# Performance work log

Hardware: AMD Instinct MI355X
Metric: run time of the kernel (lower is better)

The kernel has to match this reference:

```python
import jax, jax.numpy as jnp
import numpy as np

BATCH = 16384
IN_DIM = 256
UNITS = 256


def setup_inputs() -> dict:
    key = jax.random.key(0)
    ks = jax.random.split(key, 5)
    scale = 1.0 / np.sqrt(IN_DIM + UNITS)
    return {
        "x": jax.random.normal(ks[0], (BATCH, IN_DIM), dtype=jnp.float32),
        "prev_h": jax.random.normal(ks[1], (BATCH, UNITS), dtype=jnp.float32),
        "Wz": jax.random.normal(ks[2], (IN_DIM + UNITS, UNITS), dtype=jnp.float32) * scale,
        "bz": jnp.zeros((UNITS,), dtype=jnp.float32),
        "Wr": jax.random.normal(ks[3], (IN_DIM + UNITS, UNITS), dtype=jnp.float32) * scale,
        "br": jnp.zeros((UNITS,), dtype=jnp.float32),
        "Ws": jax.random.normal(ks[4], (IN_DIM + UNITS, UNITS), dtype=jnp.float32) * scale,
        "bs": jnp.zeros((UNITS,), dtype=jnp.float32),
    }


def reference(x, prev_h, Wz, bz, Wr, br, Ws, bs):
    # concat order matches the TF module: [prev_h, x]
    concat = jnp.concatenate([prev_h, x], axis=1)  # [B, units+in_dim]
    z = jax.nn.sigmoid(concat @ Wz + bz)
    r = jax.nn.sigmoid(concat @ Wr + br)
    concat_cand = jnp.concatenate([r * prev_h, x], axis=1)
    h_tilda = jnp.tanh(concat_cand @ Ws + bs)
    h_new = (1.0 - z) * prev_h + z * h_tilda
    return h_new
```

## Files before the change

kernel.cpp:

```cpp
#include <hip/hip_runtime.h>
#include <hip/hip_bf16.h>


#define ROWS 64

typedef float f32x4 __attribute__((ext_vector_type(4)));
typedef __bf16 bf16x8 __attribute__((ext_vector_type(8)));
typedef unsigned short us8 __attribute__((ext_vector_type(8)));
typedef unsigned short us4v __attribute__((ext_vector_type(4)));

static __device__ __forceinline__ unsigned short f2bf(float f) {
    __bf16 h = (__bf16)f;
    return __builtin_bit_cast(unsigned short, h);
}
static __device__ __forceinline__ float bf2f(unsigned short u) {
    union { unsigned u; float f; } v; v.u = ((unsigned)u) << 16;
    return v.f;
}

__global__ void pack_weights(const float* __restrict__ Wz,
                             const float* __restrict__ Wr,
                             const float* __restrict__ Ws,
                             unsigned short* __restrict__ out) {
    int gid = blockIdx.x * blockDim.x + threadIdx.x;
    int w    = gid >> 14;
    int rem  = gid & 16383;
    int kt   = rem >> 10;
    int rem2 = rem & 1023;
    int nt   = rem2 >> 6;
    int lane = rem2 & 63;
    int hi = lane >> 4, lo = lane & 15;
    const float* W = (w == 0) ? Wz : (w == 1) ? Wr : Ws;
    const float* src = W + (size_t)(kt * 32 + hi * 8) * 256 + nt * 16 + lo;
    us8 o;
#pragma unroll
    for (int j = 0; j < 8; ++j) o[j] = f2bf(src[(size_t)j * 256]);
    *(us8*)&out[(size_t)w * 131072 + (size_t)(((kt * 16 + nt) * 64 + lane) * 8)] = o;
}

__launch_bounds__(1024, 4)
__global__ void gru_main(const float* __restrict__ x,
                         const float* __restrict__ ph,
                         const float* __restrict__ bz,
                         const float* __restrict__ br,
                         const float* __restrict__ bs,
                         const unsigned short* __restrict__ Wp,
                         float* __restrict__ out) {
    __shared__ unsigned short sm[ROWS * 512];
    __shared__ unsigned short rh[ROWS * 256];

    const int tid  = threadIdx.x;
    const int lane = tid & 63;
    const int wid  = tid >> 6;
    const int brow = blockIdx.x * ROWS;

    const int l15 = lane & 15;
    const int kg  = (lane >> 4) << 3;
    const int col = wid * 16 + l15;

    const unsigned short* pz = Wp          + (size_t)((wid * 64 + lane) * 8);
    const unsigned short* pr = Wp + 131072 + (size_t)((wid * 64 + lane) * 8);
    const unsigned short* ps = Wp + 262144 + (size_t)((wid * 64 + lane) * 8);
    us8 b0n = *(const us8*)pz;
    us8 b1n = *(const us8*)pr;
    float bzc = bz[col], brc = br[col], bsc = bs[col];

#pragma unroll
    for (int it = 0; it < 4; ++it) {
        int i   = tid + it * 1024;
        int row = i >> 6;
        int c4  = (i & 63) << 2;
        int swr = (row & 7) << 3;
        float4 a = *(const float4*)&ph[(size_t)(brow + row) * 256 + c4];
        us4v u; u.x = f2bf(a.x); u.y = f2bf(a.y); u.z = f2bf(a.z); u.w = f2bf(a.w);
        *(us4v*)&sm[row * 512 + (c4 ^ swr)] = u;
    }
    __syncthreads();

    float4 xr[4];
#pragma unroll
    for (int it = 0; it < 4; ++it) {
        int i   = tid + it * 1024;
        int row = i >> 6;
        int c4  = (i & 63) << 2;
        xr[it] = *(const float4*)&x[(size_t)(brow + row) * 256 + c4];
    }

    f32x4 accz[4] = {};
    f32x4 accr[4] = {};
#pragma unroll 4
    for (int kt = 0; kt < 8; ++kt) {
        bf16x8 B0 = __builtin_bit_cast(bf16x8, b0n);
        bf16x8 B1 = __builtin_bit_cast(bf16x8, b1n);
        b0n = *(const us8*)(pz + (size_t)(kt + 1) * 8192);
        b1n = *(const us8*)(pr + (size_t)(kt + 1) * 8192);
        int ak = kt * 32 + kg;
#pragma unroll
        for (int m = 0; m < 4; ++m) {
            int arow = m * 16 + l15;
            bf16x8 a = __builtin_bit_cast(bf16x8,
                *(const us8*)&sm[arow * 512 + (ak ^ ((arow & 7) << 3))]);
            accz[m] = __builtin_amdgcn_mfma_f32_16x16x32_bf16(a, B0, accz[m], 0, 0, 0);
            accr[m] = __builtin_amdgcn_mfma_f32_16x16x32_bf16(a, B1, accr[m], 0, 0, 0);
        }
    }

#pragma unroll
    for (int it = 0; it < 4; ++it) {
        int i   = tid + it * 1024;
        int row = i >> 6;
        int c4  = (i & 63) << 2;
        int swr = (row & 7) << 3;
        us4v v; v.x = f2bf(xr[it].x); v.y = f2bf(xr[it].y);
        v.z = f2bf(xr[it].z); v.w = f2bf(xr[it].w);
        *(us4v*)&sm[row * 512 + ((256 + c4) ^ swr)] = v;
    }
    __syncthreads();

    us8 s0n = *(const us8*)(ps + (size_t)8 * 8192);
    us8 s1n = *(const us8*)(ps + (size_t)9 * 8192);

    f32x4 accs[4] = {};
#pragma unroll 4
    for (int kt = 8; kt < 16; ++kt) {
        bf16x8 B0 = __builtin_bit_cast(bf16x8, b0n);
        bf16x8 B1 = __builtin_bit_cast(bf16x8, b1n);
        bf16x8 S  = __builtin_bit_cast(bf16x8, s0n);
        s0n = s1n;
        if (kt < 15) {
            size_t no = (size_t)(kt + 1) * 8192;
            b0n = *(const us8*)(pz + no);
            b1n = *(const us8*)(pr + no);
        }
        if (kt < 14) s1n = *(const us8*)(ps + (size_t)(kt + 2) * 8192);
        int ak = kt * 32 + kg;
#pragma unroll
        for (int m = 0; m < 4; ++m) {
            int arow = m * 16 + l15;
            bf16x8 a = __builtin_bit_cast(bf16x8,
                *(const us8*)&sm[arow * 512 + (ak ^ ((arow & 7) << 3))]);
            accz[m] = __builtin_amdgcn_mfma_f32_16x16x32_bf16(a, B0, accz[m], 0, 0, 0);
            accr[m] = __builtin_amdgcn_mfma_f32_16x16x32_bf16(a, B1, accr[m], 0, 0, 0);
            accs[m] = __builtin_amdgcn_mfma_f32_16x16x32_bf16(a, S,  accs[m], 0, 0, 0);
        }
    }

    s0n = *(const us8*)ps;
    s1n = *(const us8*)(ps + 8192);

    float pst[4][4];
    const int rrow0 = (lane >> 4) * 4;
#pragma unroll
    for (int m = 0; m < 4; ++m) {
#pragma unroll
        for (int i = 0; i < 4; ++i) {
            int lrow = m * 16 + rrow0 + i;
            int cs = col ^ ((lrow & 7) << 3);
            float p = bf2f(sm[lrow * 512 + cs]);
            float z = 1.f / (1.f + __expf(-(accz[m][i] + bzc)));
            float r = 1.f / (1.f + __expf(-(accr[m][i] + brc)));
            accz[m][i] = z;
            pst[m][i]  = p;
            rh[lrow * 256 + cs] = f2bf(r * p);
        }
    }
    __syncthreads();

#pragma unroll 4
    for (int kt = 0; kt < 8; ++kt) {
        bf16x8 B = __builtin_bit_cast(bf16x8, s0n);
        s0n = s1n;
        if (kt < 6) s1n = *(const us8*)(ps + (size_t)(kt + 2) * 8192);
        int ak = kt * 32 + kg;
#pragma unroll
        for (int m = 0; m < 4; ++m) {
            int arow = m * 16 + l15;
            bf16x8 a = __builtin_bit_cast(bf16x8,
                *(const us8*)&rh[arow * 256 + (ak ^ ((arow & 7) << 3))]);
            accs[m] = __builtin_amdgcn_mfma_f32_16x16x32_bf16(a, B, accs[m], 0, 0, 0);
        }
    }

#pragma unroll
    for (int m = 0; m < 4; ++m) {
#pragma unroll
        for (int i = 0; i < 4; ++i) {
            float s = accs[m][i] + bsc;
            float e = __expf(-2.f * fabsf(s));
            float th = (1.f - e) / (1.f + e);
            th = (s < 0.f) ? -th : th;
            float z = accz[m][i];
            float p = pst[m][i];
            int grow = brow + m * 16 + rrow0 + i;
            out[(size_t)grow * 256 + col] = (1.f - z) * p + z * th;
        }
    }
}

extern "C" void kernel_launch(void* const* d_in, const int* in_sizes, int n_in,
                              void* d_out, int out_size, void* d_ws, size_t ws_size,
                              hipStream_t stream) {
    const float* x  = (const float*)d_in[0];
    const float* ph = (const float*)d_in[1];
    const float* Wz = (const float*)d_in[2];
    const float* bz = (const float*)d_in[3];
    const float* Wr = (const float*)d_in[4];
    const float* br = (const float*)d_in[5];
    const float* Ws = (const float*)d_in[6];
    const float* bs = (const float*)d_in[7];
    unsigned short* Wp = (unsigned short*)d_ws;

    hipLaunchKernelGGL(pack_weights, dim3(192), dim3(256), 0, stream, Wz, Wr, Ws, Wp);
    hipLaunchKernelGGL(gru_main, dim3(256), dim3(1024), 0, stream,
                       x, ph, bz, br, bs, Wp, (float*)d_out);
}
```

Measured before the change: 33.80 us.

## Halve row tile to 32 and give each wave two column tiles

The block tile drops from 64 to 32 rows, with 512 threads instead of 1024 and twice as many blocks. Each of the 8 waves now covers 32 output columns as two 16-column MFMA tiles, so every A fragment read from LDS feeds twice as many MFMAs. Weight prefetch is restructured to load both column tiles per k-step. This gives more blocks and better A reuse, at the cost of more weight traffic per output row and more accumulator registers per thread. The shared arrays are still sized with ROWS, so LDS use per block halves.

```diff
diff --git a/kernel.cpp b/kernel.cpp
--- a/kernel.cpp
+++ b/kernel.cpp
@@ -2,7 +2,7 @@
 #include <hip/hip_bf16.h>
 
 
-#define ROWS 64
+#define ROWS 32
 
 typedef float f32x4 __attribute__((ext_vector_type(4)));
 typedef __bf16 bf16x8 __attribute__((ext_vector_type(8)));
@@ -38,7 +38,7 @@
     *(us8*)&out[(size_t)w * 131072 + (size_t)(((kt * 16 + nt) * 64 + lane) * 8)] = o;
 }
 
-__launch_bounds__(1024, 4)
+__launch_bounds__(512, 4)
 __global__ void gru_main(const float* __restrict__ x,
                          const float* __restrict__ ph,
                          const float* __restrict__ bz,
@@ -56,18 +56,21 @@
 
     const int l15 = lane & 15;
     const int kg  = (lane >> 4) << 3;
-    const int col = wid * 16 + l15;
-
-    const unsigned short* pz = Wp          + (size_t)((wid * 64 + lane) * 8);
-    const unsigned short* pr = Wp + 131072 + (size_t)((wid * 64 + lane) * 8);
-    const unsigned short* ps = Wp + 262144 + (size_t)((wid * 64 + lane) * 8);
-    us8 b0n = *(const us8*)pz;
-    us8 b1n = *(const us8*)pr;
-    float bzc = bz[col], brc = br[col], bsc = bs[col];
+    const int c0  = wid * 32 + l15;
+    const int c1  = c0 + 16;
+
+    const unsigned short* pz = Wp          + (size_t)(wid * 128 + lane) * 8;
+    const unsigned short* pr = pz + 131072;
+    const unsigned short* ps = pz + 262144;
+    us8 z0n = *(const us8*)pz;  us8 z1n = *(const us8*)(pz + 512);
+    us8 r0n = *(const us8*)pr;  us8 r1n = *(const us8*)(pr + 512);
+    const float bz0 = bz[c0], bz1 = bz[c1];
+    const float br0 = br[c0], br1 = br[c1];
+    const float bs0 = bs[c0], bs1 = bs[c1];
 
 #pragma unroll
     for (int it = 0; it < 4; ++it) {
-        int i   = tid + it * 1024;
+        int i   = tid + it * 512;
         int row = i >> 6;
         int c4  = (i & 63) << 2;
         int swr = (row & 7) << 3;
@@ -80,34 +83,37 @@
     float4 xr[4];
 #pragma unroll
     for (int it = 0; it < 4; ++it) {
-        int i   = tid + it * 1024;
+        int i   = tid + it * 512;
         int row = i >> 6;
         int c4  = (i & 63) << 2;
         xr[it] = *(const float4*)&x[(size_t)(brow + row) * 256 + c4];
     }
 
-    f32x4 accz[4] = {};
-    f32x4 accr[4] = {};
+    f32x4 accz[2][2] = {};
+    f32x4 accr[2][2] = {};
 #pragma unroll 4
     for (int kt = 0; kt < 8; ++kt) {
-        bf16x8 B0 = __builtin_bit_cast(bf16x8, b0n);
-        bf16x8 B1 = __builtin_bit_cast(bf16x8, b1n);
-        b0n = *(const us8*)(pz + (size_t)(kt + 1) * 8192);
-        b1n = *(const us8*)(pr + (size_t)(kt + 1) * 8192);
+        bf16x8 Z0 = __builtin_bit_cast(bf16x8, z0n), Z1 = __builtin_bit_cast(bf16x8, z1n);
+        bf16x8 R0 = __builtin_bit_cast(bf16x8, r0n), R1 = __builtin_bit_cast(bf16x8, r1n);
+        size_t no = (size_t)(kt + 1) * 8192;
+        z0n = *(const us8*)(pz + no); z1n = *(const us8*)(pz + no + 512);
+        r0n = *(const us8*)(pr + no); r1n = *(const us8*)(pr + no + 512);
         int ak = kt * 32 + kg;
 #pragma unroll
-        for (int m = 0; m < 4; ++m) {
+        for (int m = 0; m < 2; ++m) {
             int arow = m * 16 + l15;
             bf16x8 a = __builtin_bit_cast(bf16x8,
                 *(const us8*)&sm[arow * 512 + (ak ^ ((arow & 7) << 3))]);
-            accz[m] = __builtin_amdgcn_mfma_f32_16x16x32_bf16(a, B0, accz[m], 0, 0, 0);
-            accr[m] = __builtin_amdgcn_mfma_f32_16x16x32_bf16(a, B1, accr[m], 0, 0, 0);
+            accz[m][0] = __builtin_amdgcn_mfma_f32_16x16x32_bf16(a, Z0, accz[m][0], 0, 0, 0);
+            accz[m][1] = __builtin_amdgcn_mfma_f32_16x16x32_bf16(a, Z1, accz[m][1], 0, 0, 0);
+            accr[m][0] = __builtin_amdgcn_mfma_f32_16x16x32_bf16(a, R0, accr[m][0], 0, 0, 0);
+            accr[m][1] = __builtin_amdgcn_mfma_f32_16x16x32_bf16(a, R1, accr[m][1], 0, 0, 0);
         }
     }
 
 #pragma unroll
     for (int it = 0; it < 4; ++it) {
-        int i   = tid + it * 1024;
+        int i   = tid + it * 512;
         int row = i >> 6;
         int c4  = (i & 63) << 2;
         int swr = (row & 7) << 3;
@@ -118,83 +124,91 @@
     __syncthreads();
 
     us8 s0n = *(const us8*)(ps + (size_t)8 * 8192);
-    us8 s1n = *(const us8*)(ps + (size_t)9 * 8192);
-
-    f32x4 accs[4] = {};
+    us8 s1n = *(const us8*)(ps + (size_t)8 * 8192 + 512);
+
+    f32x4 accs[2][2] = {};
 #pragma unroll 4
     for (int kt = 8; kt < 16; ++kt) {
-        bf16x8 B0 = __builtin_bit_cast(bf16x8, b0n);
-        bf16x8 B1 = __builtin_bit_cast(bf16x8, b1n);
-        bf16x8 S  = __builtin_bit_cast(bf16x8, s0n);
-        s0n = s1n;
+        bf16x8 Z0 = __builtin_bit_cast(bf16x8, z0n), Z1 = __builtin_bit_cast(bf16x8, z1n);
+        bf16x8 R0 = __builtin_bit_cast(bf16x8, r0n), R1 = __builtin_bit_cast(bf16x8, r1n);
+        bf16x8 S0 = __builtin_bit_cast(bf16x8, s0n), S1 = __builtin_bit_cast(bf16x8, s1n);
         if (kt < 15) {
             size_t no = (size_t)(kt + 1) * 8192;
-            b0n = *(const us8*)(pz + no);
-            b1n = *(const us8*)(pr + no);
-        }
-        if (kt < 14) s1n = *(const us8*)(ps + (size_t)(kt + 2) * 8192);
+            z0n = *(const us8*)(pz + no); z1n = *(const us8*)(pz + no + 512);
+            r0n = *(const us8*)(pr + no); r1n = *(const us8*)(pr + no + 512);
+            s0n = *(const us8*)(ps + no); s1n = *(const us8*)(ps + no + 512);
+        }
         int ak = kt * 32 + kg;
 #pragma unroll
-        for (int m = 0; m < 4; ++m) {
+        for (int m = 0; m < 2; ++m) {
             int arow = m * 16 + l15;
             bf16x8 a = __builtin_bit_cast(bf16x8,
                 *(const us8*)&sm[arow * 512 + (ak ^ ((arow & 7) << 3))]);
-            accz[m] = __builtin_amdgcn_mfma_f32_16x16x32_bf16(a, B0, accz[m], 0, 0, 0);
-            accr[m] = __builtin_amdgcn_mfma_f32_16x16x32_bf16(a, B1, accr[m], 0, 0, 0);
-            accs[m] = __builtin_amdgcn_mfma_f32_16x16x32_bf16(a, S,  accs[m], 0, 0, 0);
+            accz[m][0] = __builtin_amdgcn_mfma_f32_16x16x32_bf16(a, Z0, accz[m][0], 0, 0, 0);
+            accz[m][1] = __builtin_amdgcn_mfma_f32_16x16x32_bf16(a, Z1, accz[m][1], 0, 0, 0);
+            accr[m][0] = __builtin_amdgcn_mfma_f32_16x16x32_bf16(a, R0, accr[m][0], 0, 0, 0);
+            accr[m][1] = __builtin_amdgcn_mfma_f32_16x16x32_bf16(a, R1, accr[m][1], 0, 0, 0);
+            accs[m][0] = __builtin_amdgcn_mfma_f32_16x16x32_bf16(a, S0, accs[m][0], 0, 0, 0);
+            accs[m][1] = __builtin_amdgcn_mfma_f32_16x16x32_bf16(a, S1, accs[m][1], 0, 0, 0);
         }
     }
 
     s0n = *(const us8*)ps;
-    s1n = *(const us8*)(ps + 8192);
-
-    float pst[4][4];
+    s1n = *(const us8*)(ps + 512);
+
+    float pst[2][2][4];
     const int rrow0 = (lane >> 4) * 4;
 #pragma unroll
-    for (int m = 0; m < 4; ++m) {
-#pragma unroll
-        for (int i = 0; i < 4; ++i) {
-            int lrow = m * 16 + rrow0 + i;
-            int cs = col ^ ((lrow & 7) << 3);
-            float p = bf2f(sm[lrow * 512 + cs]);
-            float z = 1.f / (1.f + __expf(-(accz[m][i] + bzc)));
-            float r = 1.f / (1.f + __expf(-(accr[m][i] + brc)));
-            accz[m][i] = z;
-            pst[m][i]  = p;
-            rh[lrow * 256 + cs] = f2bf(r * p);
-        }
-    }
+    for (int m = 0; m < 2; ++m)
+#pragma unroll
+        for (int t = 0; t < 2; ++t)
+#pragma unroll
+            for (int i = 0; i < 4; ++i) {
+                int lrow = m * 16 + rrow0 + i;
+                int c  = t ? c1 : c0;
+                int cs = c ^ ((lrow & 7) << 3);
+                float p = bf2f(sm[lrow * 512 + cs]);
+                float z = 1.f / (1.f + __expf(-(accz[m][t][i] + (t ? bz1 : bz0))));
+                float r = 1.f / (1.f + __expf(-(accr[m][t][i] + (t ? br1 : br0))));
+                accz[m][t][i] = z;
+                pst[m][t][i]  = p;
+                rh[lrow * 256 + cs] = f2bf(r * p);
+            }
     __syncthreads();
 
 #pragma unroll 4
     for (int kt = 0; kt < 8; ++kt) {
-        bf16x8 B = __builtin_bit_cast(bf16x8, s0n);
-        s0n = s1n;
-        if (kt < 6) s1n = *(const us8*)(ps + (size_t)(kt + 2) * 8192);
+        bf16x8 S0 = __builtin_bit_cast(bf16x8, s0n), S1 = __builtin_bit_cast(bf16x8, s1n);
+        if (kt < 7) {
+            size_t no = (size_t)(kt + 1) * 8192;
+            s0n = *(const us8*)(ps + no); s1n = *(const us8*)(ps + no + 512);
+        }
         int ak = kt * 32 + kg;
 #pragma unroll
-        for (int m = 0; m < 4; ++m) {
+        for (int m = 0; m < 2; ++m) {
             int arow = m * 16 + l15;
             bf16x8 a = __builtin_bit_cast(bf16x8,
                 *(const us8*)&rh[arow * 256 + (ak ^ ((arow & 7) << 3))]);
-            accs[m] = __builtin_amdgcn_mfma_f32_16x16x32_bf16(a, B, accs[m], 0, 0, 0);
-        }
-    }
-
-#pragma unroll
-    for (int m = 0; m < 4; ++m) {
-#pragma unroll
-        for (int i = 0; i < 4; ++i) {
-            float s = accs[m][i] + bsc;
-            float e = __expf(-2.f * fabsf(s));
-            float th = (1.f - e) / (1.f + e);
-            th = (s < 0.f) ? -th : th;
-            float z = accz[m][i];
-            float p = pst[m][i];
-            int grow = brow + m * 16 + rrow0 + i;
-            out[(size_t)grow * 256 + col] = (1.f - z) * p + z * th;
-        }
-    }
+            accs[m][0] = __builtin_amdgcn_mfma_f32_16x16x32_bf16(a, S0, accs[m][0], 0, 0, 0);
+            accs[m][1] = __builtin_amdgcn_mfma_f32_16x16x32_bf16(a, S1, accs[m][1], 0, 0, 0);
+        }
+    }
+
+#pragma unroll
+    for (int m = 0; m < 2; ++m)
+#pragma unroll
+        for (int t = 0; t < 2; ++t)
+#pragma unroll
+            for (int i = 0; i < 4; ++i) {
+                float s = accs[m][t][i] + (t ? bs1 : bs0);
+                float e = __expf(-2.f * fabsf(s));
+                float th = (1.f - e) / (1.f + e);
+                th = (s < 0.f) ? -th : th;
+                float z = accz[m][t][i];
+                float p = pst[m][t][i];
+                out[(size_t)(brow + m * 16 + rrow0 + i) * 256 + (t ? c1 : c0)]
+                    = (1.f - z) * p + z * th;
+            }
 }
 
 extern "C" void kernel_launch(void* const* d_in, const int* in_sizes, int n_in,
@@ -211,6 +225,6 @@
     unsigned short* Wp = (unsigned short*)d_ws;
 
     hipLaunchKernelGGL(pack_weights, dim3(192), dim3(256), 0, stream, Wz, Wr, Ws, Wp);
-    hipLaunchKernelGGL(gru_main, dim3(256), dim3(1024), 0, stream,
+    hipLaunchKernelGGL(gru_main, dim3(512), dim3(512), 0, stream,
                        x, ph, bz, br, bs, Wp, (float*)d_out);
 }
```

New measurement: 37.90 us. +12.1%, slower.

## Fuse weight packing into main GRU kernel via cooperative grid sync

Applied to the files above, without the earlier changes.

Folds the bf16 weight-packing kernel into the main GRU kernel and launches it cooperatively, with a grid-wide barrier separating packing from the GEMM phases. This removes one kernel launch and the gap between the two kernels. In exchange it adds a grid sync and requires all 256 blocks of 1024 threads to be co-resident, which the cooperative launch must support or the launch fails.

```diff
diff --git a/kernel.cpp b/kernel.cpp
--- a/kernel.cpp
+++ b/kernel.cpp
@@ -1,5 +1,8 @@
 #include <hip/hip_runtime.h>
 #include <hip/hip_bf16.h>
+#include <hip/hip_cooperative_groups.h>
+
+namespace cg = cooperative_groups;
 
 
 #define ROWS 64
@@ -18,34 +21,17 @@
     return v.f;
 }
 
-__global__ void pack_weights(const float* __restrict__ Wz,
-                             const float* __restrict__ Wr,
-                             const float* __restrict__ Ws,
-                             unsigned short* __restrict__ out) {
-    int gid = blockIdx.x * blockDim.x + threadIdx.x;
-    int w    = gid >> 14;
-    int rem  = gid & 16383;
-    int kt   = rem >> 10;
-    int rem2 = rem & 1023;
-    int nt   = rem2 >> 6;
-    int lane = rem2 & 63;
-    int hi = lane >> 4, lo = lane & 15;
-    const float* W = (w == 0) ? Wz : (w == 1) ? Wr : Ws;
-    const float* src = W + (size_t)(kt * 32 + hi * 8) * 256 + nt * 16 + lo;
-    us8 o;
-#pragma unroll
-    for (int j = 0; j < 8; ++j) o[j] = f2bf(src[(size_t)j * 256]);
-    *(us8*)&out[(size_t)w * 131072 + (size_t)(((kt * 16 + nt) * 64 + lane) * 8)] = o;
-}
-
 __launch_bounds__(1024, 4)
-__global__ void gru_main(const float* __restrict__ x,
-                         const float* __restrict__ ph,
-                         const float* __restrict__ bz,
-                         const float* __restrict__ br,
-                         const float* __restrict__ bs,
-                         const unsigned short* __restrict__ Wp,
-                         float* __restrict__ out) {
+__global__ void gru_fused(const float* __restrict__ x,
+                          const float* __restrict__ ph,
+                          const float* __restrict__ bz,
+                          const float* __restrict__ br,
+                          const float* __restrict__ bs,
+                          const float* __restrict__ Wz,
+                          const float* __restrict__ Wr,
+                          const float* __restrict__ Ws,
+                          unsigned short* __restrict__ Wp,
+                          float* __restrict__ out) {
     __shared__ unsigned short sm[ROWS * 512];
     __shared__ unsigned short rh[ROWS * 256];
 
@@ -53,6 +39,28 @@
     const int lane = tid & 63;
     const int wid  = tid >> 6;
     const int brow = blockIdx.x * ROWS;
+
+    {
+        int gid = blockIdx.x * 1024 + tid;
+        if (gid < 49152) {
+            int w    = gid >> 14;
+            int rem  = gid & 16383;
+            int kt   = rem >> 10;
+            int rem2 = rem & 1023;
+            int nt   = rem2 >> 6;
+            int ln   = rem2 & 63;
+            int hi = ln >> 4, lo = ln & 15;
+            const float* W = (w == 0) ? Wz : (w == 1) ? Wr : Ws;
+            const float* src = W + (size_t)(kt * 32 + hi * 8) * 256 + nt * 16 + lo;
+            us8 o;
+#pragma unroll
+            for (int j = 0; j < 8; ++j) o[j] = f2bf(src[(size_t)j * 256]);
+            *(us8*)&Wp[(size_t)w * 131072
+                       + (size_t)(((kt * 16 + nt) * 64 + ln) * 8)] = o;
+        }
+    }
+    __threadfence();
+    cg::this_grid().sync();
 
     const int l15 = lane & 15;
     const int kg  = (lane >> 4) << 3;
@@ -209,8 +217,10 @@
     const float* Ws = (const float*)d_in[6];
     const float* bs = (const float*)d_in[7];
     unsigned short* Wp = (unsigned short*)d_ws;
-
-    hipLaunchKernelGGL(pack_weights, dim3(192), dim3(256), 0, stream, Wz, Wr, Ws, Wp);
-    hipLaunchKernelGGL(gru_main, dim3(256), dim3(1024), 0, stream,
-                       x, ph, bz, br, bs, Wp, (float*)d_out);
-}
+    float* outp = (float*)d_out;
+
+    void* args[] = { (void*)&x, (void*)&ph, (void*)&bz, (void*)&br, (void*)&bs,
+                     (void*)&Wz, (void*)&Wr, (void*)&Ws, (void*)&Wp, (void*)&outp };
+    hipLaunchCooperativeKernel((const void*)gru_fused, dim3(256), dim3(1024),
+                               args, 0, stream);
+}
```

Result: slower. 132.3 us (+291.3%).

## Stream prev_h into shared memory per k-tile, overlapping its loads with MFMA

Applied to the files above, without the earlier changes.

Instead of loading and converting the whole 64x256 prev_h tile before the first GEMM phase, each thread now loads float2 pieces three k-tiles ahead and writes one 32-column slice into shared memory per iteration, with a barrier per k-tile. The aim is to overlap global-load latency for prev_h with the z/r MFMA work instead of stalling before compute starts. The cost is eight block-wide barriers instead of one, plus narrower 8-byte global loads and 4-byte LDS stores.

```diff
diff --git a/kernel.cpp b/kernel.cpp
--- a/kernel.cpp
+++ b/kernel.cpp
@@ -8,6 +8,7 @@
 typedef __bf16 bf16x8 __attribute__((ext_vector_type(8)));
 typedef unsigned short us8 __attribute__((ext_vector_type(8)));
 typedef unsigned short us4v __attribute__((ext_vector_type(4)));
+typedef unsigned short us2v __attribute__((ext_vector_type(2)));
 
 static __device__ __forceinline__ unsigned short f2bf(float f) {
     __bf16 h = (__bf16)f;
@@ -65,17 +66,10 @@
     us8 b1n = *(const us8*)pr;
     float bzc = bz[col], brc = br[col], bsc = bs[col];
 
-#pragma unroll
-    for (int it = 0; it < 4; ++it) {
-        int i   = tid + it * 1024;
-        int row = i >> 6;
-        int c4  = (i & 63) << 2;
-        int swr = (row & 7) << 3;
-        float4 a = *(const float4*)&ph[(size_t)(brow + row) * 256 + c4];
-        us4v u; u.x = f2bf(a.x); u.y = f2bf(a.y); u.z = f2bf(a.z); u.w = f2bf(a.w);
-        *(us4v*)&sm[row * 512 + (c4 ^ swr)] = u;
-    }
-    __syncthreads();
+    const int srow = tid >> 4;
+    const int c2   = (tid & 15) << 1;
+    const int sswr = (srow & 7) << 3;
+    const float* phrow = ph + (size_t)(brow + srow) * 256 + c2;
 
     float4 xr[4];
 #pragma unroll
@@ -86,15 +80,29 @@
         xr[it] = *(const float4*)&x[(size_t)(brow + row) * 256 + c4];
     }
 
+    float2 sA = *(const float2*)(phrow + 0 * 32);
+    float2 sB = *(const float2*)(phrow + 1 * 32);
+    float2 sC = *(const float2*)(phrow + 2 * 32);
+
     f32x4 accz[4] = {};
     f32x4 accr[4] = {};
-#pragma unroll 4
-    for (int kt = 0; kt < 8; ++kt) {
+#pragma unroll
+    for (int j = 0; j < 8; ++j) {
+        float2 sN;
+        if (j + 3 < 8) sN = *(const float2*)(phrow + (j + 3) * 32);
+        {
+            us2v u; u.x = f2bf(sA.x); u.y = f2bf(sA.y);
+            int scol = j * 32 + c2;
+            *(us2v*)&sm[srow * 512 + (scol ^ sswr)] = u;
+        }
+        sA = sB; sB = sC; sC = sN;
+        __syncthreads();
+
         bf16x8 B0 = __builtin_bit_cast(bf16x8, b0n);
         bf16x8 B1 = __builtin_bit_cast(bf16x8, b1n);
-        b0n = *(const us8*)(pz + (size_t)(kt + 1) * 8192);
-        b1n = *(const us8*)(pr + (size_t)(kt + 1) * 8192);
-        int ak = kt * 32 + kg;
+        b0n = *(const us8*)(pz + (size_t)(j + 1) * 8192);
+        b1n = *(const us8*)(pr + (size_t)(j + 1) * 8192);
+        int ak = j * 32 + kg;
 #pragma unroll
         for (int m = 0; m < 4; ++m) {
             int arow = m * 16 + l15;
```

Result: no change. 33.51 us (-0.9%).
